# Kernel tuning notes

Hardware: AMD Instinct MI355X
Metric: run time of the kernel (lower is better)

The kernel has to match this reference:

```python
import jax, jax.numpy as jnp
import numpy as np

B, CIN, COUT, K, H, W = 8, 256, 256, 3, 128, 128


def setup_inputs() -> dict:
    key = jax.random.key(0)
    k1, k2, k3 = jax.random.split(key, 3)
    return {
        "input_vector": jax.random.normal(k1, (B, CIN, H, W), dtype=jnp.float32),
        "style_vector": jax.random.normal(k2, (B, CIN), dtype=jnp.float32),
        "weight": jax.random.normal(k3, (COUT, CIN, K, K), dtype=jnp.float32),
    }


def reference(input_vector, style_vector, weight):
    b, cin, h, w = input_vector.shape
    cout, _, k, _ = weight.shape
    # per-sample modulated weights: (b, O, I, k, k)
    ws = weight[None, :, :, :, :] * style_vector[:, None, :, None, None]
    # NOTE: faithful to source - sum over dims [1,2,3] = (O, I, kh), NOT kw.
    demod = jax.lax.rsqrt(jnp.sum(ws * ws, axis=(1, 2, 3), keepdims=True) + 1e-8)  # (b,1,1,1,k)
    ws = (ws * demod).reshape(b * cout, cin, k, k)
    x = input_vector.reshape(1, b * cin, h, w)
    # get_same_padding(W, k, dilation=1, stride=1) = (k-1)//2
    pad = ((w - 1) * (1 - 1) + 1 * (k - 1)) // 2
    out = jax.lax.conv_general_dilated(
        x, ws,
        window_strides=(1, 1),
        padding=[(pad, pad), (pad, pad)],
        feature_group_count=b,
        dimension_numbers=("NCHW", "OIHW", "NCHW"),
    )
    out = out.reshape(b, cout, h, w)
    return jax.nn.leaky_relu(out, negative_slope=0.2)
```

## Files before the change

### kernel.cpp

```cpp
#include <hip/hip_runtime.h>
#include <hip/hip_bf16.h>

#define B_    8
#define CIN   256
#define COUT  256
#define H_    128
#define W_    128
#define HP    130
#define WP    130

#define OCT   128
#define TROWS 8
#define TCOLS 32
#define XROWS 10
#define XCOLS 34
#define XCH   1360
#define XCHP  1536
#define CCS   ((size_t)COUT * CIN)

using bfrag  = __attribute__((ext_vector_type(8))) short;
using f32x16 = __attribute__((ext_vector_type(16))) float;

#define ASM_VMCNT(n) asm volatile("s_waitcnt vmcnt(" #n ")" ::: "memory")
#define ASM_LGKM0()  asm volatile("s_waitcnt lgkmcnt(0)" ::: "memory")

__device__ __forceinline__ float leaky(float v) {
    return v >= 0.f ? v : 0.2f * v;
}

__device__ __forceinline__ unsigned short to_bf16(float v) {
    __hip_bfloat16 h = __float2bfloat16(v);
    return *(unsigned short*)&h;
}

__global__ void compute_S_kernel(const float* __restrict__ weight, float* __restrict__ S) {
    const int i = blockIdx.x;
    const int t = threadIdx.x;
    const float* wp = weight + ((size_t)t * CIN + i) * 9;
    float s0 = 0.f, s1 = 0.f, s2 = 0.f;
#pragma unroll
    for (int kh = 0; kh < 3; ++kh) {
        float a = wp[kh * 3 + 0], b = wp[kh * 3 + 1], c = wp[kh * 3 + 2];
        s0 = fmaf(a, a, s0); s1 = fmaf(b, b, s1); s2 = fmaf(c, c, s2);
    }
    __shared__ float red[3][256];
    red[0][t] = s0; red[1][t] = s1; red[2][t] = s2;
    __syncthreads();
    for (int off = 128; off > 0; off >>= 1) {
        if (t < off) {
            red[0][t] += red[0][t + off];
            red[1][t] += red[1][t + off];
            red[2][t] += red[2][t + off];
        }
        __syncthreads();
    }
    if (t == 0) {
        S[i * 3 + 0] = red[0][0];
        S[i * 3 + 1] = red[1][0];
        S[i * 3 + 2] = red[2][0];
    }
}

__global__ void compute_demod_kernel(const float* __restrict__ style,
                                     const float* __restrict__ S,
                                     float* __restrict__ demod) {
    const int b = blockIdx.x;
    const int t = threadIdx.x;
    float sv = style[b * CIN + t];
    float sv2 = sv * sv;
    float s0 = sv2 * S[t * 3 + 0];
    float s1 = sv2 * S[t * 3 + 1];
    float s2 = sv2 * S[t * 3 + 2];
    __shared__ float red[3][256];
    red[0][t] = s0; red[1][t] = s1; red[2][t] = s2;
    __syncthreads();
    for (int off = 128; off > 0; off >>= 1) {
        if (t < off) {
            red[0][t] += red[0][t + off];
            red[1][t] += red[1][t + off];
            red[2][t] += red[2][t + off];
        }
        __syncthreads();
    }
    if (t == 0) {
        demod[b * 3 + 0] = rsqrtf(red[0][0] + 1e-8f);
        demod[b * 3 + 1] = rsqrtf(red[1][0] + 1e-8f);
        demod[b * 3 + 2] = rsqrtf(red[2][0] + 1e-8f);
    }
}

__global__ void compute_wmodT_kernel(const float* __restrict__ weight,
                                     const float* __restrict__ style,
                                     const float* __restrict__ demod,
                                     unsigned short* __restrict__ wT) {
    const int bx = blockIdx.x;
    const int i  = threadIdx.x;
    const int o  = bx & (COUT - 1);
    const int j  = (bx >> 8) % 9;
    const int b  = bx / (9 * COUT);
    float w = weight[((size_t)o * CIN + i) * 9 + j];
    float m = style[b * CIN + i] * demod[b * 3 + (j % 3)];
    wT[(((size_t)(b * 9 + j) * COUT + o)) * CIN + i] = to_bf16(w * m);
}

__global__ __launch_bounds__(256) void transpose_kernel(const float* __restrict__ x,
                                                        unsigned short* __restrict__ xT) {
    const int bx = blockIdx.x;
    const int h  = blockIdx.y;
    const int b  = blockIdx.z;
    const int t  = threadIdx.x;
    const int itile = (bx >> 2) * 32;

    if (h == H_) {
        const int q = bx & 3;
        for (int idx = t; idx < 129 * 4; idx += 256) {
            int px_i = idx >> 2, q4 = idx & 3;
            int p = q * 129 + px_i;
            int row, col;
            if (p < 130)      { row = 0;       col = p; }
            else if (p < 260) { row = HP - 1;  col = p - 130; }
            else if (p < 388) { row = p - 259; col = 0; }
            else              { row = p - 387; col = WP - 1; }
            size_t off = ((size_t)b * HP * WP + (size_t)row * WP + col) * CIN
                         + itile + q4 * 8;
            *(int4*)((unsigned short*)xT + off) = (int4){0, 0, 0, 0};
        }
        return;
    }

    const int wtile = (bx & 3) * 32;
    __shared__ float lt[32][33];
    {
        const int tw = t & 31, tr = t >> 5;
#pragma unroll
        for (int rr = 0; rr < 4; ++rr) {
            int il = tr + rr * 8;
            lt[il][tw] = x[(((size_t)b * CIN + itile + il) * H_ + h) * W_ + wtile + tw];
        }
    }
    __syncthreads();
    {
        const int il = t & 31, wr = t >> 5;
#pragma unroll
        for (int rr = 0; rr < 4; ++rr) {
            int wl = wr + rr * 8;
            xT[(((size_t)b * HP + (h + 1)) * WP + (wtile + wl + 1)) * CIN + itile + il] =
                to_bf16(lt[il][wl]);
        }
    }
}

__global__ __launch_bounds__(256, 2) void conv_mfma_kernel(
    const unsigned short* __restrict__ xT,
    const unsigned short* __restrict__ wT,
    float* __restrict__ out)
{
    const int tid = threadIdx.x;
    const int lin = blockIdx.x;
    const int b    = lin & 7;
    const int rest = lin >> 3;
    const int oc0  = (rest & 1) * OCT;
    const int w0   = ((rest >> 1) & 3) * TCOLS;
    const int h0   = (rest >> 3) * TROWS;

    const int wid  = tid >> 6;
    const int lane = tid & 63;
    const int wm   = wid >> 1;
    const int cw   = wid & 1;
    const int l15  = lane & 15;
    const int l31  = lane & 31;
    const int ksl  = lane >> 5;
    const int rowoff = ((lane >> 4) & 1) * 4;

    __shared__ unsigned short lds_a[2][3 * OCT * 32];
    __shared__ unsigned short lds_x[XCHP * 8];

    const unsigned short* xb = xT + ((size_t)(b * HP + h0) * WP + w0) * CIN;
    const unsigned short* wb = wT + ((size_t)(b * 9) * COUT + oc0) * CIN;

    int offA[6];
#pragma unroll
    for (int j = 0; j < 6; ++j) {
        int c    = (wid * 6 + j) * 64 + lane;
        int slot = c & 3;
        int o    = (c >> 2) & 127;
        int kh   = c >> 9;
        offA[j] = (int)((size_t)(kh * 3) * CCS) + o * CIN
                  + ((slot ^ ((o >> 1) & 3)) << 3);
    }

    f32x16 acc[2][4];
#pragma unroll
    for (int m = 0; m < 2; ++m)
#pragma unroll
        for (int n = 0; n < 4; ++n)
#pragma unroll
            for (int e = 0; e < 16; ++e) acc[m][n][e] = 0.f;

    auto stage_A = [&](unsigned short* dst, const unsigned short* wsrc) {
#pragma unroll
        for (int j = 0; j < 6; ++j) {
            __builtin_amdgcn_global_load_lds(
                (const __attribute__((address_space(1))) void*)(wsrc + offA[j]),
                (__attribute__((address_space(3))) void*)(dst + (wid * 6 + j) * 512),
                16, 0, 0);
        }
    };
    auto stage_X = [&](int i0) {
#pragma unroll
        for (int j = 0; j < 6; ++j) {
            int g  = (wid * 6 + j) * 64 + lane;
            int gg = g < XCH ? g : 0;
            int pix = gg >> 2, slot = gg & 3;
            int row = pix / XCOLS, col = pix - row * XCOLS;
            int ofx = (row * WP + col) * CIN + ((slot ^ ((col >> 1) & 3)) << 3);
            __builtin_amdgcn_global_load_lds(
                (const __attribute__((address_space(1))) void*)(xb + ofx + i0),
                (__attribute__((address_space(3))) void*)(lds_x + (wid * 6 + j) * 512),
                16, 0, 0);
        }
    };

    const int axor = (l31 >> 1) & 3;
    const int abase = (wm * 64 + l31) * 32;

    auto compute = [&](int kw, const unsigned short* ab) {
        const int col  = cw * 16 + l15 + kw;
        const int bxor = (col >> 1) & 3;
        const unsigned short* bp0 =
            lds_x + ((rowoff) * XCOLS + col) * 32 + (((0 * 2 + ksl) ^ bxor) << 3);
        const unsigned short* bp1 =
            lds_x + ((rowoff) * XCOLS + col) * 32 + (((1 * 2 + ksl) ^ bxor) << 3);

        bfrag aF[3][2][2];
#pragma unroll
        for (int kh = 0; kh < 3; ++kh)
#pragma unroll
            for (int m = 0; m < 2; ++m)
#pragma unroll
                for (int ks = 0; ks < 2; ++ks)
                    aF[kh][m][ks] = *(const bfrag*)(ab + kh * (OCT * 32) + abase
                                      + m * (32 * 32) + (((ks * 2 + ksl) ^ axor) << 3));

        bfrag bs[2][2];
        bs[0][0] = *(const bfrag*)(bp0);
        bs[0][1] = *(const bfrag*)(bp1);

        __builtin_amdgcn_s_setprio(1);
#pragma unroll
        for (int r = 0; r < 6; ++r) {
            if (r < 5) {
                bs[(r + 1) & 1][0] = *(const bfrag*)(bp0 + (size_t)(r + 1) * XCOLS * 32);
                bs[(r + 1) & 1][1] = *(const bfrag*)(bp1 + (size_t)(r + 1) * XCOLS * 32);
            }
#pragma unroll
            for (int kh = 0; kh < 3; ++kh) {
                const int np = r - kh;
                if (np >= 0 && np < 4) {
#pragma unroll
                    for (int m = 0; m < 2; ++m) {
                        acc[m][np] = __builtin_amdgcn_mfma_f32_32x32x16_bf16(
                            aF[kh][m][0], bs[r & 1][0], acc[m][np], 0, 0, 0);
                        acc[m][np] = __builtin_amdgcn_mfma_f32_32x32x16_bf16(
                            aF[kh][m][1], bs[r & 1][1], acc[m][np], 0, 0, 0);
                    }
                }
            }
        }
        __builtin_amdgcn_s_setprio(0);
    };

    stage_X(0);
    stage_A(lds_a[0], wb);
    ASM_VMCNT(0);
    __builtin_amdgcn_s_barrier();
    __builtin_amdgcn_sched_barrier(0);

#pragma unroll 1
    for (int c = 0; c < 8; ++c) {
        unsigned short* pa = lds_a[c & 1];
        unsigned short* pb = lds_a[(c & 1) ^ 1];
        const size_t i0  = (size_t)c * 32;
        const size_t i0n = (size_t)((c + 1) & 7) * 32;

        stage_A(pb, wb + 1 * CCS + i0);
        ASM_VMCNT(6);
        __builtin_amdgcn_s_barrier();
        __builtin_amdgcn_sched_barrier(0);
        compute(0, pa);
        ASM_LGKM0(); ASM_VMCNT(0);
        __builtin_amdgcn_s_barrier();
        __builtin_amdgcn_sched_barrier(0);
        stage_A(pa, wb + 2 * CCS + i0);
        compute(1, pb);
        ASM_LGKM0(); ASM_VMCNT(0);
        __builtin_amdgcn_s_barrier();
        __builtin_amdgcn_sched_barrier(0);
        stage_A(pb, wb + i0n);
        compute(2, pa);
        ASM_LGKM0(); ASM_VMCNT(0);
        __builtin_amdgcn_s_barrier();
        __builtin_amdgcn_sched_barrier(0);
        if (c < 7) stage_X((int)i0n);
    }
    ASM_VMCNT(0);

#pragma unroll
    for (int m = 0; m < 2; ++m) {
#pragma unroll
        for (int np = 0; np < 4; ++np) {
            int h = h0 + np + rowoff;
            int w = w0 + cw * 16 + l15;
#pragma unroll
            for (int r = 0; r < 16; ++r) {
                int oc = oc0 + wm * 64 + m * 32 + ((r & 3) + 8 * (r >> 2) + 4 * ksl);
                out[(((size_t)b * COUT + oc) * H_ + h) * W_ + w] = leaky(acc[m][np][r]);
            }
        }
    }
}

extern "C" void kernel_launch(void* const* d_in, const int* in_sizes, int n_in,
                              void* d_out, int out_size, void* d_ws, size_t ws_size,
                              hipStream_t stream) {
    const float* x      = (const float*)d_in[0];
    const float* style  = (const float*)d_in[1];
    const float* weight = (const float*)d_in[2];
    float* out = (float*)d_out;

    float* S     = (float*)d_ws;
    float* demod = (float*)((char*)d_ws + 4096);
    unsigned short* wT = (unsigned short*)((char*)d_ws + 8192);
    unsigned short* xT = (unsigned short*)((char*)d_ws + 9445376);

    compute_S_kernel<<<CIN, 256, 0, stream>>>(weight, S);
    compute_demod_kernel<<<B_, 256, 0, stream>>>(style, S, demod);
    compute_wmodT_kernel<<<B_ * 9 * COUT, 256, 0, stream>>>(weight, style, demod, wT);
    transpose_kernel<<<dim3(32, H_ + 1, B_), 256, 0, stream>>>(x, xT);

    conv_mfma_kernel<<<dim3(1024), 256, 0, stream>>>(xT, wT, out);
}
```

Measured before the change: 202.5 us.

## Prefetch A fragments into registers across kw stages, reswizzle X LDS, vectorize wmodT

The conv kernel now loads the next kw stage's A fragments from LDS into registers inside the MFMA loop, so LDS reads overlap compute. The A staging schedule is reworked so each buffer is refilled one stage ahead, and an extra barrier is added after staging X. The X LDS swizzle also XORs a row-dependent bit to reduce bank conflicts between the two row halves. Separately, the weight-modulation kernel writes 8 bf16 values per thread with an int4 store, cutting its block count. The risks are higher register pressure and more barriers.

```diff
diff --git a/kernel.cpp b/kernel.cpp
--- a/kernel.cpp
+++ b/kernel.cpp
@@ -23,6 +23,9 @@
 
 #define ASM_VMCNT(n) asm volatile("s_waitcnt vmcnt(" #n ")" ::: "memory")
 #define ASM_LGKM0()  asm volatile("s_waitcnt lgkmcnt(0)" ::: "memory")
+#define BAR()  do { __builtin_amdgcn_s_barrier(); __builtin_amdgcn_sched_barrier(0); } while (0)
+
+#define SWZX(row, col) ((((col) >> 1) & 3) ^ ((((row) >> 2) & 1) << 1))
 
 __device__ __forceinline__ float leaky(float v) {
     return v >= 0.f ? v : 0.2f * v;
@@ -94,13 +97,25 @@
                                      const float* __restrict__ demod,
                                      unsigned short* __restrict__ wT) {
     const int bx = blockIdx.x;
-    const int i  = threadIdx.x;
-    const int o  = bx & (COUT - 1);
-    const int j  = (bx >> 8) % 9;
-    const int b  = bx / (9 * COUT);
-    float w = weight[((size_t)o * CIN + i) * 9 + j];
-    float m = style[b * CIN + i] * demod[b * 3 + (j % 3)];
-    wT[(((size_t)(b * 9 + j) * COUT + o)) * CIN + i] = to_bf16(w * m);
+    const int og = bx & 31;
+    const int j  = (bx >> 5) % 9;
+    const int b  = bx / (9 * 32);
+    const int t  = threadIdx.x;
+    const int o  = og * 8 + (t >> 5);
+    const int i0 = (t & 31) * 8;
+    const float dm = demod[b * 3 + (j % 3)];
+    unsigned int u[4];
+#pragma unroll
+    for (int q = 0; q < 4; ++q) {
+        int i = i0 + q * 2;
+        float w0 = weight[((size_t)o * CIN + i) * 9 + j];
+        float w1 = weight[((size_t)o * CIN + i + 1) * 9 + j];
+        unsigned int lo = to_bf16(w0 * style[b * CIN + i] * dm);
+        unsigned int hi = to_bf16(w1 * style[b * CIN + i + 1] * dm);
+        u[q] = lo | (hi << 16);
+    }
+    int4 v = make_int4(u[0], u[1], u[2], u[3]);
+    *(int4*)&wT[((size_t)(b * 9 + j) * COUT + o) * CIN + i0] = v;
 }
 
 __global__ __launch_bounds__(256) void transpose_kernel(const float* __restrict__ x,
@@ -170,7 +185,8 @@
     const int l15  = lane & 15;
     const int l31  = lane & 31;
     const int ksl  = lane >> 5;
-    const int rowoff = ((lane >> 4) & 1) * 4;
+    const int rp   = (lane >> 4) & 1;
+    const int rowoff = rp * 4;
 
     __shared__ unsigned short lds_a[2][3 * OCT * 32];
     __shared__ unsigned short lds_x[XCHP * 8];
@@ -213,7 +229,7 @@
             int gg = g < XCH ? g : 0;
             int pix = gg >> 2, slot = gg & 3;
             int row = pix / XCOLS, col = pix - row * XCOLS;
-            int ofx = (row * WP + col) * CIN + ((slot ^ ((col >> 1) & 3)) << 3);
+            int ofx = (row * WP + col) * CIN + ((slot ^ SWZX(row, col)) << 3);
             __builtin_amdgcn_global_load_lds(
                 (const __attribute__((address_space(1))) void*)(xb + ofx + i0),
                 (__attribute__((address_space(3))) void*)(lds_x + (wid * 6 + j) * 512),
@@ -221,18 +237,12 @@
         }
     };
 
-    const int axor = (l31 >> 1) & 3;
+    const int axor  = (l31 >> 1) & 3;
     const int abase = (wm * 64 + l31) * 32;
 
-    auto compute = [&](int kw, const unsigned short* ab) {
-        const int col  = cw * 16 + l15 + kw;
-        const int bxor = (col >> 1) & 3;
-        const unsigned short* bp0 =
-            lds_x + ((rowoff) * XCOLS + col) * 32 + (((0 * 2 + ksl) ^ bxor) << 3);
-        const unsigned short* bp1 =
-            lds_x + ((rowoff) * XCOLS + col) * 32 + (((1 * 2 + ksl) ^ bxor) << 3);
-
-        bfrag aF[3][2][2];
+    bfrag aF[3][2][2];
+
+    auto loadA = [&](const unsigned short* ab) {
 #pragma unroll
         for (int kh = 0; kh < 3; ++kh)
 #pragma unroll
@@ -241,17 +251,36 @@
                 for (int ks = 0; ks < 2; ++ks)
                     aF[kh][m][ks] = *(const bfrag*)(ab + kh * (OCT * 32) + abase
                                       + m * (32 * 32) + (((ks * 2 + ksl) ^ axor) << 3));
+    };
+
+    const int colB  = cw * 16 + l15;
+
+    auto compute = [&](int kw, const unsigned short* abn) {
+        const int col  = colB + kw;
+        const int cx   = (col >> 1) & 3;
+        const unsigned short* bpA[2];
+        const unsigned short* bpB[2];
+#pragma unroll
+        for (int ks = 0; ks < 2; ++ks) {
+            int slotA = ((ks * 2 + ksl) ^ cx ^ (rp << 1));
+            int slotB = ((ks * 2 + ksl) ^ cx ^ ((rp ^ 1) << 1));
+            bpA[ks] = lds_x + ((size_t)(rowoff * XCOLS) + col) * 32 + (slotA << 3);
+            bpB[ks] = lds_x + ((size_t)(rowoff * XCOLS) + col) * 32 + (slotB << 3);
+        }
 
         bfrag bs[2][2];
-        bs[0][0] = *(const bfrag*)(bp0);
-        bs[0][1] = *(const bfrag*)(bp1);
+        bs[0][0] = *(const bfrag*)(bpA[0]);
+        bs[0][1] = *(const bfrag*)(bpA[1]);
 
         __builtin_amdgcn_s_setprio(1);
 #pragma unroll
         for (int r = 0; r < 6; ++r) {
             if (r < 5) {
-                bs[(r + 1) & 1][0] = *(const bfrag*)(bp0 + (size_t)(r + 1) * XCOLS * 32);
-                bs[(r + 1) & 1][1] = *(const bfrag*)(bp1 + (size_t)(r + 1) * XCOLS * 32);
+                const int rn = r + 1;
+#pragma unroll
+                for (int ks = 0; ks < 2; ++ks)
+                    bs[rn & 1][ks] = *(const bfrag*)(
+                        (rn < 4 ? bpA[ks] : bpB[ks]) + (size_t)rn * XCOLS * 32);
             }
 #pragma unroll
             for (int kh = 0; kh < 3; ++kh) {
@@ -266,6 +295,15 @@
                     }
                 }
             }
+            if (r >= 3) {
+                const int kh = r - 3;
+#pragma unroll
+                for (int m = 0; m < 2; ++m)
+#pragma unroll
+                    for (int ks = 0; ks < 2; ++ks)
+                        aF[kh][m][ks] = *(const bfrag*)(abn + kh * (OCT * 32) + abase
+                                          + m * (32 * 32) + (((ks * 2 + ksl) ^ axor) << 3));
+            }
         }
         __builtin_amdgcn_s_setprio(0);
     };
@@ -273,35 +311,41 @@
     stage_X(0);
     stage_A(lds_a[0], wb);
     ASM_VMCNT(0);
-    __builtin_amdgcn_s_barrier();
-    __builtin_amdgcn_sched_barrier(0);
+    BAR();
+    loadA(lds_a[0]);
+    ASM_LGKM0();
+    BAR();
+    stage_A(lds_a[1], wb + 1 * CCS);
+    ASM_VMCNT(0);
+    BAR();
 
 #pragma unroll 1
     for (int c = 0; c < 8; ++c) {
-        unsigned short* pa = lds_a[c & 1];
-        unsigned short* pb = lds_a[(c & 1) ^ 1];
+        unsigned short* be = lds_a[c & 1];
+        unsigned short* bo = lds_a[(c & 1) ^ 1];
         const size_t i0  = (size_t)c * 32;
         const size_t i0n = (size_t)((c + 1) & 7) * 32;
 
-        stage_A(pb, wb + 1 * CCS + i0);
-        ASM_VMCNT(6);
-        __builtin_amdgcn_s_barrier();
+        stage_A(be, wb + 2 * CCS + i0);
         __builtin_amdgcn_sched_barrier(0);
-        compute(0, pa);
+        compute(0, bo);
         ASM_LGKM0(); ASM_VMCNT(0);
-        __builtin_amdgcn_s_barrier();
+        BAR();
+        stage_A(bo, wb + i0n);
         __builtin_amdgcn_sched_barrier(0);
-        stage_A(pa, wb + 2 * CCS + i0);
-        compute(1, pb);
+        compute(1, be);
         ASM_LGKM0(); ASM_VMCNT(0);
-        __builtin_amdgcn_s_barrier();
+        BAR();
+        stage_A(be, wb + 1 * CCS + i0n);
         __builtin_amdgcn_sched_barrier(0);
-        stage_A(pb, wb + i0n);
-        compute(2, pa);
+        compute(2, bo);
         ASM_LGKM0(); ASM_VMCNT(0);
-        __builtin_amdgcn_s_barrier();
-        __builtin_amdgcn_sched_barrier(0);
-        if (c < 7) stage_X((int)i0n);
+        BAR();
+        if (c < 7) {
+            stage_X((int)i0n);
+            ASM_VMCNT(0);
+            BAR();
+        }
     }
     ASM_VMCNT(0);
 
@@ -335,7 +379,7 @@
 
     compute_S_kernel<<<CIN, 256, 0, stream>>>(weight, S);
     compute_demod_kernel<<<B_, 256, 0, stream>>>(style, S, demod);
-    compute_wmodT_kernel<<<B_ * 9 * COUT, 256, 0, stream>>>(weight, style, demod, wT);
+    compute_wmodT_kernel<<<B_ * 9 * 32, 256, 0, stream>>>(weight, style, demod, wT);
     transpose_kernel<<<dim3(32, H_ + 1, B_), 256, 0, stream>>>(x, xT);
 
     conv_mfma_kernel<<<dim3(1024), 256, 0, stream>>>(xT, wT, out);
```

Result: faster. 197.3 us (-2.6%).
